# Kernel optimization log

Hardware: AMD Instinct MI355X
Metric: run time of the kernel (lower is better)

## Reference

```python
import jax, jax.numpy as jnp
import numpy as np

N_CENTER, N_NEAR, N_STEPK, N_HOPS = 512, 32, 10, 2
FEAT_NAMES = ["xyz_fea", "pmt_fea", "mad_fea", "dim_fea", "nor_fea", "loc_fea", "fea"]


def pairwise_sqdist(x):
    # x: [B,N,C] -> [B,N,N]
    xx = jnp.sum(x * x, axis=-1)
    return xx[:, :, None] + xx[:, None, :] - 2.0 * jnp.einsum('bnc,bmc->bnm', x, x)


def surface_knn(x, n_near, n_stepk, n_hops=N_HOPS):
    # Iterative surface-KNN: build a step-KNN graph with n_stepk neighbors,
    # expand the neighborhood n_hops times (neighbor-of-neighbor union), then
    # pick the n_near nearest points among the reachable candidate set.
    d = pairwise_sqdist(x)                      # [B,N,N]
    B, N, _ = d.shape
    _, nbr = jax.lax.top_k(-d, n_stepk + 1)     # step neighbors (incl. self)
    b_idx = jnp.arange(B)[:, None, None]
    r_idx = jnp.arange(N)[None, :, None]
    adj = jnp.zeros((B, N, N), jnp.bool_).at[b_idx, r_idx, nbr].set(True)
    reach = adj
    adj_f = adj.astype(jnp.float32)
    for _ in range(n_hops):
        reach = (jnp.einsum('bij,bjk->bik', reach.astype(jnp.float32), adj_f) > 0) | adj
    dm = jnp.where(reach, d, jnp.inf)
    _, idx = jax.lax.top_k(-dm, n_near)         # [B,N,n_near], nearest reachable
    return idx


def fps(x, n_center):
    # Farthest point sampling in the C-dim feature space (dim=dim in source).
    B, N, _ = x.shape
    d = pairwise_sqdist(x)
    barange = jnp.arange(B)

    def step(carry, _):
        mind, prev = carry
        mind = jnp.minimum(mind, d[barange, prev])   # [B,N]
        nxt = jnp.argmax(mind, axis=-1).astype(jnp.int32)
        return (mind, nxt), nxt

    init = (jnp.full((B, N), jnp.inf, jnp.float32), jnp.zeros((B,), jnp.int32))
    _, rest = jax.lax.scan(step, init, None, length=n_center - 1)  # [S-1,B]
    idx = jnp.concatenate([jnp.zeros((1, B), jnp.int32), rest], axis=0)
    return idx.T                                   # [B,S]


def branch(center, grouped, wq, bq, wk, bk, wv, bv, w1, b1, w2, b2):
    # center: [B,S,C], grouped: [B,S,K,C]
    C = center.shape[-1]
    q = center @ wq + bq                           # [B,S,C]
    k = grouped @ wk + bk                          # [B,S,K,C]
    v = grouped @ wv + bv
    scores = jnp.einsum('bsc,bskc->bsk', q, k) / jnp.sqrt(jnp.float32(C))
    attn = jax.nn.softmax(scores, axis=-1)
    out = jnp.einsum('bsk,bskc->bsc', attn, v)     # attention pooling -> [B,S,C]
    h = jax.nn.relu(out @ w1 + b1)                 # MLP (C -> Cout -> Cout)
    return jax.nn.relu(h @ w2 + b2)


def setup_inputs() -> dict:
    key = jax.random.key(0)
    ks = jax.random.split(key, 16)
    B, N, C, CO = 8, 2048, 128, 256
    inp = {}
    for i, name in enumerate(FEAT_NAMES):
        inp[name] = jax.random.normal(ks[i], (B, N, C), jnp.float32)
    s = np.float32(1.0 / np.sqrt(C))
    so = np.float32(1.0 / np.sqrt(CO))
    inp['aw_q'] = jax.random.normal(ks[7], (7, C, C), jnp.float32) * s
    inp['ab_q'] = jnp.zeros((7, C), jnp.float32)
    inp['aw_k'] = jax.random.normal(ks[8], (7, C, C), jnp.float32) * s
    inp['ab_k'] = jnp.zeros((7, C), jnp.float32)
    inp['aw_v'] = jax.random.normal(ks[9], (7, C, C), jnp.float32) * s
    inp['ab_v'] = jnp.zeros((7, C), jnp.float32)
    inp['mw1'] = jax.random.normal(ks[10], (7, C, CO), jnp.float32) * s
    inp['mb1'] = jnp.zeros((7, CO), jnp.float32)
    inp['mw2'] = jax.random.normal(ks[11], (7, CO, CO), jnp.float32) * so
    inp['mb2'] = jnp.zeros((7, CO), jnp.float32)
    return inp


def reference(xyz_fea, pmt_fea, mad_fea, dim_fea, nor_fea, loc_fea, fea,
              aw_q, ab_q, aw_k, ab_k, aw_v, ab_v, mw1, mb1, mw2, mb2):
    B = xyz_fea.shape[0]
    feats = jnp.stack([xyz_fea, pmt_fea, mad_fea, dim_fea, nor_fea, loc_fea, fea], 0)  # [7,B,N,C]
    idx_all = surface_knn(xyz_fea, N_NEAR, N_STEPK)      # [B,N,K]
    fps_idx = fps(xyz_fea, N_CENTER)                     # [B,S]
    b2 = jnp.arange(B)[:, None]                          # [B,1]
    b3 = jnp.arange(B)[:, None, None]                    # [B,1,1]
    centers = feats[:, b2, fps_idx]                      # [7,B,S,C]
    idx = idx_all[b2, fps_idx]                           # [B,S,K]
    grouped = feats[:, b3, idx]                          # [7,B,S,K,C]
    outs = jax.vmap(branch)(centers, grouped, aw_q, ab_q, aw_k, ab_k,
                            aw_v, ab_v, mw1, mb1, mw2, mb2)  # [7,B,S,CO]
    return tuple(outs[i] for i in range(7))
```

## Files before the change

### kernel.cpp

```cpp
#include <hip/hip_runtime.h>
#include <hip/hip_bf16.h>
#include <math.h>

constexpr int BATCH = 8;
constexpr int NPTS  = 2048;
constexpr int CH    = 128;
constexpr int CHO   = 256;
constexpr int NCEN  = 512;
constexpr int NNEI  = 32;
constexpr int NTOP  = 11;
constexpr int NW    = 64;

struct Ptr7 { const float* p[7]; };

__global__ __launch_bounds__(256) void xx_kernel(const float* __restrict__ x,
                                                 float* __restrict__ xx) {
    int p = blockIdx.x * 256 + threadIdx.x;
    if (p >= BATCH * NPTS) return;
    const float4* xr = (const float4*)(x + (size_t)p * CH);
    float s = 0.f;
#pragma unroll
    for (int i = 0; i < CH / 4; i++) {
        float4 v = xr[i];
        s += v.x * v.x + v.y * v.y + v.z * v.z + v.w * v.w;
    }
    xx[p] = s;
}

__global__ __launch_bounds__(256) void dmat_kernel(const float* __restrict__ x,
                                                   const float* __restrict__ xx,
                                                   float* __restrict__ D) {
    __shared__ float As[32][68];
    __shared__ float Bs[32][68];
    int bz = blockIdx.z;
    int i0 = blockIdx.y * 64, j0 = blockIdx.x * 64;
    const float* X = x + (size_t)bz * NPTS * CH;
    int t = threadIdx.x, tx = t & 15, ty = t >> 4;
    int lr = t >> 3, lc = (t & 7) * 4;
    const float* ai0 = X + (size_t)(i0 + lr) * CH;
    const float* ai1 = X + (size_t)(i0 + lr + 32) * CH;
    const float* bj0 = X + (size_t)(j0 + lr) * CH;
    const float* bj1 = X + (size_t)(j0 + lr + 32) * CH;
    float acc[4][4] = {};
    for (int kc = 0; kc < CH; kc += 32) {
        float4 a0 = *(const float4*)(ai0 + kc + lc);
        float4 a1 = *(const float4*)(ai1 + kc + lc);
        float4 b0 = *(const float4*)(bj0 + kc + lc);
        float4 b1 = *(const float4*)(bj1 + kc + lc);
        __syncthreads();
        As[lc + 0][lr] = a0.x; As[lc + 1][lr] = a0.y; As[lc + 2][lr] = a0.z; As[lc + 3][lr] = a0.w;
        As[lc + 0][lr + 32] = a1.x; As[lc + 1][lr + 32] = a1.y; As[lc + 2][lr + 32] = a1.z; As[lc + 3][lr + 32] = a1.w;
        Bs[lc + 0][lr] = b0.x; Bs[lc + 1][lr] = b0.y; Bs[lc + 2][lr] = b0.z; Bs[lc + 3][lr] = b0.w;
        Bs[lc + 0][lr + 32] = b1.x; Bs[lc + 1][lr + 32] = b1.y; Bs[lc + 2][lr + 32] = b1.z; Bs[lc + 3][lr + 32] = b1.w;
        __syncthreads();
#pragma unroll
        for (int kk = 0; kk < 32; kk++) {
            float4 av = *(const float4*)&As[kk][ty * 4];
            float4 bv = *(const float4*)&Bs[kk][tx * 4];
            float a[4] = {av.x, av.y, av.z, av.w};
            float b[4] = {bv.x, bv.y, bv.z, bv.w};
#pragma unroll
            for (int i = 0; i < 4; i++)
#pragma unroll
                for (int j = 0; j < 4; j++) acc[i][j] += a[i] * b[j];
        }
    }
    const float* xxb = xx + bz * NPTS;
    float xi[4], xj[4];
#pragma unroll
    for (int i = 0; i < 4; i++) xi[i] = xxb[i0 + ty * 4 + i];
#pragma unroll
    for (int j = 0; j < 4; j++) xj[j] = xxb[j0 + tx * 4 + j];
#pragma unroll
    for (int i = 0; i < 4; i++) {
        float4 o;
        o.x = xi[i] + xj[0] - 2.f * acc[i][0];
        o.y = xi[i] + xj[1] - 2.f * acc[i][1];
        o.z = xi[i] + xj[2] - 2.f * acc[i][2];
        o.w = xi[i] + xj[3] - 2.f * acc[i][3];
        *(float4*)(D + ((size_t)bz * NPTS + i0 + ty * 4 + i) * NPTS + j0 + tx * 4) = o;
    }
}

__global__ __launch_bounds__(256) void knn_fps_kernel(const float* __restrict__ D,
                                                      unsigned int* __restrict__ adj,
                                                      int* __restrict__ fps_idx) {
    if (blockIdx.x < BATCH) {
        int lane = threadIdx.x;
        if (lane >= 64) return;
        int b = blockIdx.x;
        float mind[32];
#pragma unroll
        for (int r = 0; r < 32; r++) mind[r] = INFINITY;
        int prev = 0;
        if (lane == 0) fps_idx[b * NCEN] = 0;
        const float* Db = D + (size_t)b * NPTS * NPTS;
        for (int s = 1; s < NCEN; s++) {
            const float4* rowp = (const float4*)(Db + (size_t)prev * NPTS);
            float4 v0 = rowp[lane + 0 * 64];
            float4 v1 = rowp[lane + 1 * 64];
            float4 v2 = rowp[lane + 2 * 64];
            float4 v3 = rowp[lane + 3 * 64];
            float4 v4 = rowp[lane + 4 * 64];
            float4 v5 = rowp[lane + 5 * 64];
            float4 v6 = rowp[lane + 6 * 64];
            float4 v7 = rowp[lane + 7 * 64];
            float bv = -INFINITY; int bj = NPTS;
            float4 vv[8] = {v0, v1, v2, v3, v4, v5, v6, v7};
#pragma unroll
            for (int k = 0; k < 8; k++) {
                int j0 = 4 * (lane + 64 * k);
                float m0 = fminf(mind[4 * k + 0], vv[k].x); mind[4 * k + 0] = m0;
                float m1 = fminf(mind[4 * k + 1], vv[k].y); mind[4 * k + 1] = m1;
                float m2 = fminf(mind[4 * k + 2], vv[k].z); mind[4 * k + 2] = m2;
                float m3 = fminf(mind[4 * k + 3], vv[k].w); mind[4 * k + 3] = m3;
                if (m0 > bv) { bv = m0; bj = j0 + 0; }
                if (m1 > bv) { bv = m1; bj = j0 + 1; }
                if (m2 > bv) { bv = m2; bj = j0 + 2; }
                if (m3 > bv) { bv = m3; bj = j0 + 3; }
            }
#pragma unroll
            for (int off = 32; off > 0; off >>= 1) {
                float ov = __shfl_xor(bv, off);
                int oj = __shfl_xor(bj, off);
                if (ov > bv || (ov == bv && oj < bj)) { bv = ov; bj = oj; }
            }
            if (lane == 0) fps_idx[b * NCEN + s] = bj;
            prev = bj;
        }
        return;
    }
    __shared__ float row[NPTS];
    __shared__ float rv[256];
    __shared__ int ri[256];
    __shared__ int picks[NTOP + 1];
    int rid = blockIdx.x - BATCH;
    const float* Dr = D + (size_t)rid * NPTS;
    int t = threadIdx.x;
    float4* rp = (float4*)row;
    rp[t] = ((const float4*)Dr)[t];
    rp[t + 256] = ((const float4*)Dr)[t + 256];
    __syncthreads();
    for (int it = 0; it < NTOP; it++) {
        float bv = row[t];
        int bi = t;
#pragma unroll
        for (int k = 1; k < 8; k++) {
            int j = t + (k << 8);
            float v = row[j];
            if (v < bv) { bv = v; bi = j; }
        }
        rv[t] = bv; ri[t] = bi;
        __syncthreads();
        for (int off = 128; off > 0; off >>= 1) {
            if (t < off) {
                float ov = rv[t + off]; int oi = ri[t + off];
                if (ov < rv[t] || (ov == rv[t] && oi < ri[t])) { rv[t] = ov; ri[t] = oi; }
            }
            __syncthreads();
        }
        if (t == 0) { picks[it] = ri[0]; row[ri[0]] = INFINITY; }
        __syncthreads();
    }
    if (t < NW) {
        unsigned w = 0;
#pragma unroll
        for (int p = 0; p < NTOP; p++) {
            int j = picks[p];
            if ((j >> 5) == t) w |= 1u << (j & 31);
        }
        adj[(size_t)rid * NW + t] = w;
    }
}

__global__ void make_gather(const int* __restrict__ fps_idx, int* __restrict__ gatherC) {
    int r = blockIdx.x * 256 + threadIdx.x;
    if (r >= BATCH * NCEN) return;
    int b = r >> 9, s = r & 511;
    gatherC[r] = b * NPTS + fps_idx[b * NCEN + s];
}

__global__ __launch_bounds__(256) void reach_top32_kernel(const unsigned int* __restrict__ adj,
                                                          const float* __restrict__ D,
                                                          const int* __restrict__ fps_idx,
                                                          int* __restrict__ idx_sel) {
    __shared__ unsigned adjw[NW], R1[NW], R2[NW];
    __shared__ int lst[NPTS];
    __shared__ float dst[NPTS];
    __shared__ int cnt;
    __shared__ float rv[256];
    __shared__ int rj[256], rp[256];
    __shared__ int sel[NNEI];
    int s = blockIdx.x, b = blockIdx.y, t = threadIdx.x;
    int i = fps_idx[b * NCEN + s];
    const unsigned* arow = adj + ((size_t)(b * NPTS + i)) * NW;
    if (t < NW) { adjw[t] = arow[t]; R1[t] = arow[t]; }
    if (t == 0) cnt = 0;
    __syncthreads();
    if (t < NW) {
        unsigned w = adjw[t];
        while (w) { int bb = __ffs(w) - 1; w &= w - 1; int p = atomicAdd(&cnt, 1); lst[p] = t * 32 + bb; }
    }
    __syncthreads();
    int n1 = cnt;
    {
        int g = t >> 6, lane = t & 63;
        for (int p = g; p < n1; p += 4) {
            unsigned aw = adj[((size_t)(b * NPTS + lst[p])) * NW + lane];
            atomicOr(&R1[lane], aw);
        }
    }
    __syncthreads();
    if (t == 0) cnt = 0;
    __syncthreads();
    if (t < NW) {
        unsigned w = R1[t];
        while (w) { int bb = __ffs(w) - 1; w &= w - 1; int p = atomicAdd(&cnt, 1); lst[p] = t * 32 + bb; }
        R2[t] = adjw[t];
    }
    __syncthreads();
    int n2 = cnt;
    {
        int g = t >> 6, lane = t & 63;
        for (int p = g; p < n2; p += 4) {
            unsigned aw = adj[((size_t)(b * NPTS + lst[p])) * NW + lane];
            atomicOr(&R2[lane], aw);
        }
    }
    __syncthreads();
    if (t == 0) cnt = 0;
    __syncthreads();
    const float* Dr = D + (size_t)(b * NPTS + i) * NPTS;
    if (t < NW) {
        unsigned w = R2[t];
        while (w) {
            int bb = __ffs(w) - 1; w &= w - 1;
            int j = t * 32 + bb;
            int p = atomicAdd(&cnt, 1);
            lst[p] = j; dst[p] = Dr[j];
        }
    }
    __syncthreads();
    int L = cnt;
    int nsel = L < NNEI ? L : NNEI;
    for (int r = 0; r < nsel; r++) {
        float bv = INFINITY; int bj = 0x7fffffff, bp = -1;
        for (int p = t; p < L; p += 256) {
            float v = dst[p]; int j = lst[p];
            if (v < bv || (v == bv && j < bj)) { bv = v; bj = j; bp = p; }
        }
        rv[t] = bv; rj[t] = bj; rp[t] = bp;
        __syncthreads();
        for (int off = 128; off > 0; off >>= 1) {
            if (t < off) {
                if (rv[t + off] < rv[t] || (rv[t + off] == rv[t] && rj[t + off] < rj[t])) {
                    rv[t] = rv[t + off]; rj[t] = rj[t + off]; rp[t] = rp[t + off];
                }
            }
            __syncthreads();
        }
        if (t == 0) { sel[r] = rj[0]; dst[rp[0]] = INFINITY; }
        __syncthreads();
    }
    if (t == 0 && nsel < NNEI) {
        int r = nsel;
        for (int j = 0; j < NPTS && r < NNEI; j++)
            if (!((R2[j >> 5] >> (j & 31)) & 1)) sel[r++] = j;
    }
    __syncthreads();
    if (t < NNEI) idx_sel[((size_t)(b * NCEN + s)) * NNEI + t] = sel[t];
}

template <int KSIZE, bool RELU>
__device__ __forceinline__ void gemm_tile64(const float* __restrict__ A, int lda,
                                            const int* __restrict__ gather,
                                            const float* __restrict__ W, int ldw,
                                            const float* __restrict__ bias,
                                            float* __restrict__ Out, int ldo) {
    __shared__ float As[32][68];
    __shared__ float Ws[32][68];
    int t = threadIdx.x;
    int tx = t & 15, ty = t >> 4;
    int lr = t >> 3, lc = (t & 7) * 4;
    const float* ar0 = A + (size_t)(gather ? gather[lr] : lr) * lda;
    const float* ar1 = A + (size_t)(gather ? gather[lr + 32] : lr + 32) * lda;
    float acc[4][4] = {};
    for (int kc = 0; kc < KSIZE; kc += 32) {
        float4 a0 = *(const float4*)(ar0 + kc + lc);
        float4 a1 = *(const float4*)(ar1 + kc + lc);
        float4 w0 = *(const float4*)(W + (size_t)(kc + lr) * ldw + lc);
        float4 w1 = *(const float4*)(W + (size_t)(kc + lr) * ldw + lc + 32);
        __syncthreads();
        As[lc + 0][lr] = a0.x; As[lc + 1][lr] = a0.y; As[lc + 2][lr] = a0.z; As[lc + 3][lr] = a0.w;
        As[lc + 0][lr + 32] = a1.x; As[lc + 1][lr + 32] = a1.y; As[lc + 2][lr + 32] = a1.z; As[lc + 3][lr + 32] = a1.w;
        *(float4*)&Ws[lr][lc] = w0;
        *(float4*)&Ws[lr][lc + 32] = w1;
        __syncthreads();
#pragma unroll
        for (int kk = 0; kk < 32; kk++) {
            float4 av = *(const float4*)&As[kk][ty * 4];
            float4 wv = *(const float4*)&Ws[kk][tx * 4];
            float a[4] = {av.x, av.y, av.z, av.w};
            float w[4] = {wv.x, wv.y, wv.z, wv.w};
#pragma unroll
            for (int i = 0; i < 4; i++)
#pragma unroll
                for (int j = 0; j < 4; j++) acc[i][j] += a[i] * w[j];
        }
    }
#pragma unroll
    for (int i = 0; i < 4; i++) {
        int r = ty * 4 + i;
        float4 o;
        o.x = acc[i][0] + bias[tx * 4 + 0];
        o.y = acc[i][1] + bias[tx * 4 + 1];
        o.z = acc[i][2] + bias[tx * 4 + 2];
        o.w = acc[i][3] + bias[tx * 4 + 3];
        if (RELU) {
            o.x = fmaxf(o.x, 0.f); o.y = fmaxf(o.y, 0.f);
            o.z = fmaxf(o.z, 0.f); o.w = fmaxf(o.w, 0.f);
        }
        *(float4*)(Out + (size_t)r * ldo + tx * 4) = o;
    }
}

__global__ __launch_bounds__(256) void kvproj_kernel(Ptr7 feats, const float* __restrict__ awk,
                                                     const float* __restrict__ abk,
                                                     const float* __restrict__ awv,
                                                     const float* __restrict__ abv,
                                                     float* __restrict__ ktab,
                                                     float* __restrict__ vtab) {
    int v = blockIdx.z, ct = blockIdx.y, rt = blockIdx.x;
    bool isv = ct >= 2;
    int c2 = ct & 1;
    const float* A = feats.p[v] + (size_t)rt * 64 * CH;
    const float* W = (isv ? awv : awk) + (size_t)v * CH * CH + c2 * 64;
    const float* bias = (isv ? abv : abk) + v * CH + c2 * 64;
    float* Out = (isv ? vtab : ktab) + (size_t)v * (BATCH * NPTS) * CH + (size_t)rt * 64 * CH + c2 * 64;
    gemm_tile64<CH, false>(A, CH, nullptr, W, CH, bias, Out, CH);
}

__global__ __launch_bounds__(256) void qproj_kernel(Ptr7 feats, const float* __restrict__ awq,
                                                    const float* __restrict__ abq,
                                                    const int* __restrict__ gatherC,
                                                    float* __restrict__ qtab) {
    int v = blockIdx.z, ct = blockIdx.y, rt = blockIdx.x;
    gemm_tile64<CH, false>(feats.p[v], CH, gatherC + rt * 64,
                           awq + (size_t)v * CH * CH + ct * 64, CH,
                           abq + v * CH + ct * 64,
                           qtab + ((size_t)v * (BATCH * NCEN) + rt * 64) * CH + ct * 64, CH);
}

__global__ __launch_bounds__(256) void mlp1_kernel(const float* __restrict__ otab,
                                                   const float* __restrict__ mw1,
                                                   const float* __restrict__ mb1,
                                                   float* __restrict__ htab) {
    int v = blockIdx.z, ct = blockIdx.y, rt = blockIdx.x;
    gemm_tile64<CH, true>(otab + ((size_t)v * (BATCH * NCEN) + rt * 64) * CH, CH, nullptr,
                          mw1 + (size_t)v * CH * CHO + ct * 64, CHO,
                          mb1 + v * CHO + ct * 64,
                          htab + ((size_t)v * (BATCH * NCEN) + rt * 64) * CHO + ct * 64, CHO);
}

__global__ __launch_bounds__(256) void mlp2_kernel(const float* __restrict__ htab,
                                                   const float* __restrict__ mw2,
                                                   const float* __restrict__ mb2,
                                                   float* __restrict__ out) {
    int v = blockIdx.z, ct = blockIdx.y, rt = blockIdx.x;
    gemm_tile64<CHO, true>(htab + ((size_t)v * (BATCH * NCEN) + rt * 64) * CHO, CHO, nullptr,
                           mw2 + (size_t)v * CHO * CHO + ct * 64, CHO,
                           mb2 + v * CHO + ct * 64,
                           out + ((size_t)v * (BATCH * NCEN) + rt * 64) * CHO + ct * 64, CHO);
}

__global__ __launch_bounds__(256) void attn_kernel(const float* __restrict__ qtab,
                                                   const float* __restrict__ ktab,
                                                   const float* __restrict__ vtab,
                                                   const int* __restrict__ idx_sel,
                                                   float* __restrict__ otab) {
    __shared__ float q_s[4][CH];
    __shared__ float attn_s[4][NNEI];
    __shared__ int jj_s[4][NNEI];
    int v = blockIdx.y;
    int t = threadIdx.x, w = t >> 6, lane = t & 63;
    int cg = blockIdx.x * 4 + w;
    int b = cg >> 9, s = cg & 511;
    const float* qr = qtab + ((size_t)v * (BATCH * NCEN) + cg) * CH;
    *(float2*)&q_s[w][lane * 2] = *(const float2*)(qr + lane * 2);
    if (lane < NNEI) jj_s[w][lane] = idx_sel[((size_t)(b * NCEN + s)) * NNEI + lane];
    __syncthreads();
    if (lane < NNEI) {
        int j = jj_s[w][lane];
        const float* kr = ktab + ((size_t)v * (BATCH * NPTS) + b * NPTS + j) * CH;
        float acc = 0.f;
#pragma unroll
        for (int c4 = 0; c4 < CH / 4; c4++) {
            float4 qv = *(const float4*)&q_s[w][c4 * 4];
            float4 kv = *(const float4*)(kr + c4 * 4);
            acc += qv.x * kv.x + qv.y * kv.y + qv.z * kv.z + qv.w * kv.w;
        }
        float sc = acc * 0.08838834764831845f;
        float m = sc;
#pragma unroll
        for (int off = 16; off > 0; off >>= 1) m = fmaxf(m, __shfl_xor(m, off, 32));
        float e = expf(sc - m);
        float sum = e;
#pragma unroll
        for (int off = 16; off > 0; off >>= 1) sum += __shfl_xor(sum, off, 32);
        attn_s[w][lane] = e / sum;
    }
    __syncthreads();
    float2 o = {0.f, 0.f};
    const float* vbase = vtab + ((size_t)v * (BATCH * NPTS) + b * NPTS) * CH;
    for (int tt = 0; tt < NNEI; tt++) {
        int j = jj_s[w][tt];
        float a = attn_s[w][tt];
        float2 vv = *(const float2*)(vbase + (size_t)j * CH + lane * 2);
        o.x += a * vv.x;
        o.y += a * vv.y;
    }
    *(float2*)(otab + ((size_t)v * (BATCH * NCEN) + cg) * CH + lane * 2) = o;
}

extern "C" void kernel_launch(void* const* d_in, const int* in_sizes, int n_in,
                              void* d_out, int out_size, void* d_ws, size_t ws_size,
                              hipStream_t stream) {
    (void)in_sizes; (void)n_in; (void)out_size;
    Ptr7 feats;
    for (int i = 0; i < 7; i++) feats.p[i] = (const float*)d_in[i];
    const float* awq = (const float*)d_in[7];
    const float* abq = (const float*)d_in[8];
    const float* awk = (const float*)d_in[9];
    const float* abk = (const float*)d_in[10];
    const float* awv = (const float*)d_in[11];
    const float* abv = (const float*)d_in[12];
    const float* mw1 = (const float*)d_in[13];
    const float* mb1 = (const float*)d_in[14];
    const float* mw2 = (const float*)d_in[15];
    const float* mb2 = (const float*)d_in[16];
    const float* xyz = feats.p[0];

    char* ws = (char*)d_ws;
    size_t SZ_D = (size_t)BATCH * NPTS * NPTS * 4;
    float* D = (float*)ws;
    float* ktab = (float*)ws;
    float* vtab = (float*)(ws + (size_t)7 * BATCH * NPTS * CH * 4);
    size_t off = SZ_D;
    float* xx = (float*)(ws + off); off += (size_t)BATCH * NPTS * 4;
    unsigned* adjb = (unsigned*)(ws + off); off += (size_t)BATCH * NPTS * NW * 4;
    int* fpsidx = (int*)(ws + off); off += (size_t)BATCH * NCEN * 4;
    int* idxsel = (int*)(ws + off); off += (size_t)BATCH * NCEN * NNEI * 4;
    int* gatherC = (int*)(ws + off); off += (size_t)BATCH * NCEN * 4;
    float* qtab = (float*)(ws + off); off += (size_t)7 * BATCH * NCEN * CH * 4;
    float* otab = (float*)(ws + off); off += (size_t)7 * BATCH * NCEN * CH * 4;
    float* htab = (float*)(ws + off); off += (size_t)7 * BATCH * NCEN * CHO * 4;
    if (ws_size < off) return;

    xx_kernel<<<dim3((BATCH * NPTS + 255) / 256), dim3(256), 0, stream>>>(xyz, xx);
    dmat_kernel<<<dim3(NPTS / 64, NPTS / 64, BATCH), dim3(256), 0, stream>>>(xyz, xx, D);
    knn_fps_kernel<<<dim3(BATCH + BATCH * NPTS), dim3(256), 0, stream>>>(D, adjb, fpsidx);
    make_gather<<<dim3((BATCH * NCEN + 255) / 256), dim3(256), 0, stream>>>(fpsidx, gatherC);
    reach_top32_kernel<<<dim3(NCEN, BATCH), dim3(256), 0, stream>>>(adjb, D, fpsidx, idxsel);
    kvproj_kernel<<<dim3(BATCH * NPTS / 64, 4, 7), dim3(256), 0, stream>>>(feats, awk, abk, awv, abv, ktab, vtab);
    qproj_kernel<<<dim3(BATCH * NCEN / 64, 2, 7), dim3(256), 0, stream>>>(feats, awq, abq, gatherC, qtab);
    attn_kernel<<<dim3(BATCH * NCEN / 4, 7), dim3(256), 0, stream>>>(qtab, ktab, vtab, idxsel, otab);
    mlp1_kernel<<<dim3(BATCH * NCEN / 64, 4, 7), dim3(256), 0, stream>>>(otab, mw1, mb1, htab);
    mlp2_kernel<<<dim3(BATCH * NCEN / 64, 4, 7), dim3(256), 0, stream>>>(htab, mw2, mb2, (float*)d_out);
}
```

Measured before the change: 1.162 ms.

## Fuse K/V projection into the FPS/KNN kernel to overlap with serial FPS

Adds K/V projection GEMM tiles as extra blocks in the kernel that runs FPS and step-KNN, so the projection work can fill the GPU while the few serial FPS blocks run. Because of this, K/V tables get separate workspace instead of aliasing the distance matrix, with a fallback to the old separate launch when workspace is too small. The FPS min-distance array moves from registers to shared memory, and all GEMMs now use a passed-in shared buffer. Risks: the active path depends on workspace size, and FPS picks up shared-memory traffic on its critical path.

```diff
diff --git a/kernel.cpp b/kernel.cpp
--- a/kernel.cpp
+++ b/kernel.cpp
@@ -10,6 +10,7 @@
 constexpr int NNEI  = 32;
 constexpr int NTOP  = 11;
 constexpr int NW    = 64;
+constexpr int SMEM_BYTES = 17408;
 
 struct Ptr7 { const float* p[7]; };
 
@@ -82,42 +83,108 @@
     }
 }
 
-__global__ __launch_bounds__(256) void knn_fps_kernel(const float* __restrict__ D,
-                                                      unsigned int* __restrict__ adj,
-                                                      int* __restrict__ fps_idx) {
+template <int KSIZE, bool RELU>
+__device__ __forceinline__ void gemm_tile64(char* smem,
+                                            const float* __restrict__ A, int lda,
+                                            const int* __restrict__ gather,
+                                            const float* __restrict__ W, int ldw,
+                                            const float* __restrict__ bias,
+                                            float* __restrict__ Out, int ldo) {
+    float (*As)[68] = (float(*)[68])smem;
+    float (*Ws)[68] = (float(*)[68])(smem + 32 * 68 * 4);
+    int t = threadIdx.x;
+    int tx = t & 15, ty = t >> 4;
+    int lr = t >> 3, lc = (t & 7) * 4;
+    const float* ar0 = A + (size_t)(gather ? gather[lr] : lr) * lda;
+    const float* ar1 = A + (size_t)(gather ? gather[lr + 32] : lr + 32) * lda;
+    float acc[4][4] = {};
+    for (int kc = 0; kc < KSIZE; kc += 32) {
+        float4 a0 = *(const float4*)(ar0 + kc + lc);
+        float4 a1 = *(const float4*)(ar1 + kc + lc);
+        float4 w0 = *(const float4*)(W + (size_t)(kc + lr) * ldw + lc);
+        float4 w1 = *(const float4*)(W + (size_t)(kc + lr) * ldw + lc + 32);
+        __syncthreads();
+        As[lc + 0][lr] = a0.x; As[lc + 1][lr] = a0.y; As[lc + 2][lr] = a0.z; As[lc + 3][lr] = a0.w;
+        As[lc + 0][lr + 32] = a1.x; As[lc + 1][lr + 32] = a1.y; As[lc + 2][lr + 32] = a1.z; As[lc + 3][lr + 32] = a1.w;
+        *(float4*)&Ws[lr][lc] = w0;
+        *(float4*)&Ws[lr][lc + 32] = w1;
+        __syncthreads();
+#pragma unroll
+        for (int kk = 0; kk < 32; kk++) {
+            float4 av = *(const float4*)&As[kk][ty * 4];
+            float4 wv = *(const float4*)&Ws[kk][tx * 4];
+            float a[4] = {av.x, av.y, av.z, av.w};
+            float w[4] = {wv.x, wv.y, wv.z, wv.w};
+#pragma unroll
+            for (int i = 0; i < 4; i++)
+#pragma unroll
+                for (int j = 0; j < 4; j++) acc[i][j] += a[i] * w[j];
+        }
+    }
+#pragma unroll
+    for (int i = 0; i < 4; i++) {
+        int r = ty * 4 + i;
+        float4 o;
+        o.x = acc[i][0] + bias[tx * 4 + 0];
+        o.y = acc[i][1] + bias[tx * 4 + 1];
+        o.z = acc[i][2] + bias[tx * 4 + 2];
+        o.w = acc[i][3] + bias[tx * 4 + 3];
+        if (RELU) {
+            o.x = fmaxf(o.x, 0.f); o.y = fmaxf(o.y, 0.f);
+            o.z = fmaxf(o.z, 0.f); o.w = fmaxf(o.w, 0.f);
+        }
+        *(float4*)(Out + (size_t)r * ldo + tx * 4) = o;
+    }
+}
+
+__global__ __launch_bounds__(256) void fused_front_kernel(const float* __restrict__ D,
+                                                          unsigned int* __restrict__ adj,
+                                                          int* __restrict__ fps_idx,
+                                                          Ptr7 feats,
+                                                          const float* __restrict__ awk,
+                                                          const float* __restrict__ abk,
+                                                          const float* __restrict__ awv,
+                                                          const float* __restrict__ abv,
+                                                          float* __restrict__ ktab,
+                                                          float* __restrict__ vtab) {
+    __shared__ __align__(16) char smem[SMEM_BYTES];
     if (blockIdx.x < BATCH) {
         int lane = threadIdx.x;
         if (lane >= 64) return;
         int b = blockIdx.x;
-        float mind[32];
-#pragma unroll
-        for (int r = 0; r < 32; r++) mind[r] = INFINITY;
+        float4* mp = (float4*)smem;
+        float4 inf4 = {INFINITY, INFINITY, INFINITY, INFINITY};
+#pragma unroll
+        for (int k = 0; k < 8; k++) mp[lane + 64 * k] = inf4;
         int prev = 0;
         if (lane == 0) fps_idx[b * NCEN] = 0;
         const float* Db = D + (size_t)b * NPTS * NPTS;
         for (int s = 1; s < NCEN; s++) {
             const float4* rowp = (const float4*)(Db + (size_t)prev * NPTS);
-            float4 v0 = rowp[lane + 0 * 64];
-            float4 v1 = rowp[lane + 1 * 64];
-            float4 v2 = rowp[lane + 2 * 64];
-            float4 v3 = rowp[lane + 3 * 64];
-            float4 v4 = rowp[lane + 4 * 64];
-            float4 v5 = rowp[lane + 5 * 64];
-            float4 v6 = rowp[lane + 6 * 64];
-            float4 v7 = rowp[lane + 7 * 64];
+            float4 g0 = rowp[lane + 0 * 64];
+            float4 g1 = rowp[lane + 1 * 64];
+            float4 g2 = rowp[lane + 2 * 64];
+            float4 g3 = rowp[lane + 3 * 64];
+            float4 g4 = rowp[lane + 4 * 64];
+            float4 g5 = rowp[lane + 5 * 64];
+            float4 g6 = rowp[lane + 6 * 64];
+            float4 g7 = rowp[lane + 7 * 64];
+            float4 g[8] = {g0, g1, g2, g3, g4, g5, g6, g7};
             float bv = -INFINITY; int bj = NPTS;
-            float4 vv[8] = {v0, v1, v2, v3, v4, v5, v6, v7};
 #pragma unroll
             for (int k = 0; k < 8; k++) {
-                int j0 = 4 * (lane + 64 * k);
-                float m0 = fminf(mind[4 * k + 0], vv[k].x); mind[4 * k + 0] = m0;
-                float m1 = fminf(mind[4 * k + 1], vv[k].y); mind[4 * k + 1] = m1;
-                float m2 = fminf(mind[4 * k + 2], vv[k].z); mind[4 * k + 2] = m2;
-                float m3 = fminf(mind[4 * k + 3], vv[k].w); mind[4 * k + 3] = m3;
-                if (m0 > bv) { bv = m0; bj = j0 + 0; }
-                if (m1 > bv) { bv = m1; bj = j0 + 1; }
-                if (m2 > bv) { bv = m2; bj = j0 + 2; }
-                if (m3 > bv) { bv = m3; bj = j0 + 3; }
+                int li = lane + 64 * k;
+                float4 m = mp[li];
+                m.x = fminf(m.x, g[k].x);
+                m.y = fminf(m.y, g[k].y);
+                m.z = fminf(m.z, g[k].z);
+                m.w = fminf(m.w, g[k].w);
+                mp[li] = m;
+                int j0 = 4 * li;
+                if (m.x > bv) { bv = m.x; bj = j0 + 0; }
+                if (m.y > bv) { bv = m.y; bj = j0 + 1; }
+                if (m.z > bv) { bv = m.z; bj = j0 + 2; }
+                if (m.w > bv) { bv = m.w; bj = j0 + 3; }
             }
 #pragma unroll
             for (int off = 32; off > 0; off >>= 1) {
@@ -130,46 +197,62 @@
         }
         return;
     }
-    __shared__ float row[NPTS];
-    __shared__ float rv[256];
-    __shared__ int ri[256];
-    __shared__ int picks[NTOP + 1];
-    int rid = blockIdx.x - BATCH;
-    const float* Dr = D + (size_t)rid * NPTS;
-    int t = threadIdx.x;
-    float4* rp = (float4*)row;
-    rp[t] = ((const float4*)Dr)[t];
-    rp[t + 256] = ((const float4*)Dr)[t + 256];
-    __syncthreads();
-    for (int it = 0; it < NTOP; it++) {
-        float bv = row[t];
-        int bi = t;
-#pragma unroll
-        for (int k = 1; k < 8; k++) {
-            int j = t + (k << 8);
-            float v = row[j];
-            if (v < bv) { bv = v; bi = j; }
-        }
-        rv[t] = bv; ri[t] = bi;
-        __syncthreads();
-        for (int off = 128; off > 0; off >>= 1) {
-            if (t < off) {
-                float ov = rv[t + off]; int oi = ri[t + off];
-                if (ov < rv[t] || (ov == rv[t] && oi < ri[t])) { rv[t] = ov; ri[t] = oi; }
+    if (blockIdx.x < BATCH + BATCH * NPTS) {
+        float* row = (float*)smem;
+        float* rv = row + NPTS;
+        int* ri = (int*)(rv + 256);
+        int* picks = ri + 256;
+        int rid = blockIdx.x - BATCH;
+        const float* Dr = D + (size_t)rid * NPTS;
+        int t = threadIdx.x;
+        float4* rp = (float4*)row;
+        rp[t] = ((const float4*)Dr)[t];
+        rp[t + 256] = ((const float4*)Dr)[t + 256];
+        __syncthreads();
+        for (int it = 0; it < NTOP; it++) {
+            float bv = row[t];
+            int bi = t;
+#pragma unroll
+            for (int k = 1; k < 8; k++) {
+                int j = t + (k << 8);
+                float v = row[j];
+                if (v < bv) { bv = v; bi = j; }
             }
+            rv[t] = bv; ri[t] = bi;
             __syncthreads();
-        }
-        if (t == 0) { picks[it] = ri[0]; row[ri[0]] = INFINITY; }
-        __syncthreads();
-    }
-    if (t < NW) {
-        unsigned w = 0;
-#pragma unroll
-        for (int p = 0; p < NTOP; p++) {
-            int j = picks[p];
-            if ((j >> 5) == t) w |= 1u << (j & 31);
-        }
-        adj[(size_t)rid * NW + t] = w;
+            for (int off = 128; off > 0; off >>= 1) {
+                if (t < off) {
+                    float ov = rv[t + off]; int oi = ri[t + off];
+                    if (ov < rv[t] || (ov == rv[t] && oi < ri[t])) { rv[t] = ov; ri[t] = oi; }
+                }
+                __syncthreads();
+            }
+            if (t == 0) { picks[it] = ri[0]; row[ri[0]] = INFINITY; }
+            __syncthreads();
+        }
+        if (t < NW) {
+            unsigned w = 0;
+#pragma unroll
+            for (int p = 0; p < NTOP; p++) {
+                int j = picks[p];
+                if ((j >> 5) == t) w |= 1u << (j & 31);
+            }
+            adj[(size_t)rid * NW + t] = w;
+        }
+        return;
+    }
+    {
+        int id = blockIdx.x - BATCH - BATCH * NPTS;
+        int rt = id & 255;
+        int ct = (id >> 8) & 3;
+        int v = id >> 10;
+        bool isv = ct >= 2;
+        int c2 = ct & 1;
+        const float* A = feats.p[v] + (size_t)rt * 64 * CH;
+        const float* W = (isv ? awv : awk) + (size_t)v * CH * CH + c2 * 64;
+        const float* bias = (isv ? abv : abk) + v * CH + c2 * 64;
+        float* Out = (isv ? vtab : ktab) + (size_t)v * (BATCH * NPTS) * CH + (size_t)rt * 64 * CH + c2 * 64;
+        gemm_tile64<CH, false>(smem, A, CH, nullptr, W, CH, bias, Out, CH);
     }
 }
 
@@ -271,65 +354,13 @@
     if (t < NNEI) idx_sel[((size_t)(b * NCEN + s)) * NNEI + t] = sel[t];
 }
 
-template <int KSIZE, bool RELU>
-__device__ __forceinline__ void gemm_tile64(const float* __restrict__ A, int lda,
-                                            const int* __restrict__ gather,
-                                            const float* __restrict__ W, int ldw,
-                                            const float* __restrict__ bias,
-                                            float* __restrict__ Out, int ldo) {
-    __shared__ float As[32][68];
-    __shared__ float Ws[32][68];
-    int t = threadIdx.x;
-    int tx = t & 15, ty = t >> 4;
-    int lr = t >> 3, lc = (t & 7) * 4;
-    const float* ar0 = A + (size_t)(gather ? gather[lr] : lr) * lda;
-    const float* ar1 = A + (size_t)(gather ? gather[lr + 32] : lr + 32) * lda;
-    float acc[4][4] = {};
-    for (int kc = 0; kc < KSIZE; kc += 32) {
-        float4 a0 = *(const float4*)(ar0 + kc + lc);
-        float4 a1 = *(const float4*)(ar1 + kc + lc);
-        float4 w0 = *(const float4*)(W + (size_t)(kc + lr) * ldw + lc);
-        float4 w1 = *(const float4*)(W + (size_t)(kc + lr) * ldw + lc + 32);
-        __syncthreads();
-        As[lc + 0][lr] = a0.x; As[lc + 1][lr] = a0.y; As[lc + 2][lr] = a0.z; As[lc + 3][lr] = a0.w;
-        As[lc + 0][lr + 32] = a1.x; As[lc + 1][lr + 32] = a1.y; As[lc + 2][lr + 32] = a1.z; As[lc + 3][lr + 32] = a1.w;
-        *(float4*)&Ws[lr][lc] = w0;
-        *(float4*)&Ws[lr][lc + 32] = w1;
-        __syncthreads();
-#pragma unroll
-        for (int kk = 0; kk < 32; kk++) {
-            float4 av = *(const float4*)&As[kk][ty * 4];
-            float4 wv = *(const float4*)&Ws[kk][tx * 4];
-            float a[4] = {av.x, av.y, av.z, av.w};
-            float w[4] = {wv.x, wv.y, wv.z, wv.w};
-#pragma unroll
-            for (int i = 0; i < 4; i++)
-#pragma unroll
-                for (int j = 0; j < 4; j++) acc[i][j] += a[i] * w[j];
-        }
-    }
-#pragma unroll
-    for (int i = 0; i < 4; i++) {
-        int r = ty * 4 + i;
-        float4 o;
-        o.x = acc[i][0] + bias[tx * 4 + 0];
-        o.y = acc[i][1] + bias[tx * 4 + 1];
-        o.z = acc[i][2] + bias[tx * 4 + 2];
-        o.w = acc[i][3] + bias[tx * 4 + 3];
-        if (RELU) {
-            o.x = fmaxf(o.x, 0.f); o.y = fmaxf(o.y, 0.f);
-            o.z = fmaxf(o.z, 0.f); o.w = fmaxf(o.w, 0.f);
-        }
-        *(float4*)(Out + (size_t)r * ldo + tx * 4) = o;
-    }
-}
-
 __global__ __launch_bounds__(256) void kvproj_kernel(Ptr7 feats, const float* __restrict__ awk,
                                                      const float* __restrict__ abk,
                                                      const float* __restrict__ awv,
                                                      const float* __restrict__ abv,
                                                      float* __restrict__ ktab,
                                                      float* __restrict__ vtab) {
+    __shared__ __align__(16) char smem[SMEM_BYTES];
     int v = blockIdx.z, ct = blockIdx.y, rt = blockIdx.x;
     bool isv = ct >= 2;
     int c2 = ct & 1;
@@ -337,15 +368,16 @@
     const float* W = (isv ? awv : awk) + (size_t)v * CH * CH + c2 * 64;
     const float* bias = (isv ? abv : abk) + v * CH + c2 * 64;
     float* Out = (isv ? vtab : ktab) + (size_t)v * (BATCH * NPTS) * CH + (size_t)rt * 64 * CH + c2 * 64;
-    gemm_tile64<CH, false>(A, CH, nullptr, W, CH, bias, Out, CH);
+    gemm_tile64<CH, false>(smem, A, CH, nullptr, W, CH, bias, Out, CH);
 }
 
 __global__ __launch_bounds__(256) void qproj_kernel(Ptr7 feats, const float* __restrict__ awq,
                                                     const float* __restrict__ abq,
                                                     const int* __restrict__ gatherC,
                                                     float* __restrict__ qtab) {
+    __shared__ __align__(16) char smem[SMEM_BYTES];
     int v = blockIdx.z, ct = blockIdx.y, rt = blockIdx.x;
-    gemm_tile64<CH, false>(feats.p[v], CH, gatherC + rt * 64,
+    gemm_tile64<CH, false>(smem, feats.p[v], CH, gatherC + rt * 64,
                            awq + (size_t)v * CH * CH + ct * 64, CH,
                            abq + v * CH + ct * 64,
                            qtab + ((size_t)v * (BATCH * NCEN) + rt * 64) * CH + ct * 64, CH);
@@ -355,8 +387,9 @@
                                                    const float* __restrict__ mw1,
                                                    const float* __restrict__ mb1,
                                                    float* __restrict__ htab) {
+    __shared__ __align__(16) char smem[SMEM_BYTES];
     int v = blockIdx.z, ct = blockIdx.y, rt = blockIdx.x;
-    gemm_tile64<CH, true>(otab + ((size_t)v * (BATCH * NCEN) + rt * 64) * CH, CH, nullptr,
+    gemm_tile64<CH, true>(smem, otab + ((size_t)v * (BATCH * NCEN) + rt * 64) * CH, CH, nullptr,
                           mw1 + (size_t)v * CH * CHO + ct * 64, CHO,
                           mb1 + v * CHO + ct * 64,
                           htab + ((size_t)v * (BATCH * NCEN) + rt * 64) * CHO + ct * 64, CHO);
@@ -366,8 +399,9 @@
                                                    const float* __restrict__ mw2,
                                                    const float* __restrict__ mb2,
                                                    float* __restrict__ out) {
+    __shared__ __align__(16) char smem[SMEM_BYTES];
     int v = blockIdx.z, ct = blockIdx.y, rt = blockIdx.x;
-    gemm_tile64<CHO, true>(htab + ((size_t)v * (BATCH * NCEN) + rt * 64) * CHO, CHO, nullptr,
+    gemm_tile64<CHO, true>(smem, htab + ((size_t)v * (BATCH * NCEN) + rt * 64) * CHO, CHO, nullptr,
                            mw2 + (size_t)v * CHO * CHO + ct * 64, CHO,
                            mb2 + v * CHO + ct * 64,
                            out + ((size_t)v * (BATCH * NCEN) + rt * 64) * CHO + ct * 64, CHO);
@@ -442,9 +476,8 @@
 
     char* ws = (char*)d_ws;
     size_t SZ_D = (size_t)BATCH * NPTS * NPTS * 4;
+    size_t SZ_KV = (size_t)7 * BATCH * NPTS * CH * 4;
     float* D = (float*)ws;
-    float* ktab = (float*)ws;
-    float* vtab = (float*)(ws + (size_t)7 * BATCH * NPTS * CH * 4);
     size_t off = SZ_D;
     float* xx = (float*)(ws + off); off += (size_t)BATCH * NPTS * 4;
     unsigned* adjb = (unsigned*)(ws + off); off += (size_t)BATCH * NPTS * NW * 4;
@@ -455,13 +488,25 @@
     float* otab = (float*)(ws + off); off += (size_t)7 * BATCH * NCEN * CH * 4;
     float* htab = (float*)(ws + off); off += (size_t)7 * BATCH * NCEN * CHO * 4;
     if (ws_size < off) return;
+    bool kv_sep = (ws_size >= off + 2 * SZ_KV);
+    float *ktab, *vtab;
+    if (kv_sep) {
+        ktab = (float*)(ws + off); off += SZ_KV;
+        vtab = (float*)(ws + off); off += SZ_KV;
+    } else {
+        ktab = (float*)ws;
+        vtab = (float*)(ws + SZ_KV);
+    }
 
     xx_kernel<<<dim3((BATCH * NPTS + 255) / 256), dim3(256), 0, stream>>>(xyz, xx);
     dmat_kernel<<<dim3(NPTS / 64, NPTS / 64, BATCH), dim3(256), 0, stream>>>(xyz, xx, D);
-    knn_fps_kernel<<<dim3(BATCH + BATCH * NPTS), dim3(256), 0, stream>>>(D, adjb, fpsidx);
+    int fused_blocks = BATCH + BATCH * NPTS + (kv_sep ? 7 * 4 * (BATCH * NPTS / 64) : 0);
+    fused_front_kernel<<<dim3(fused_blocks), dim3(256), 0, stream>>>(D, adjb, fpsidx, feats,
+                                                                     awk, abk, awv, abv, ktab, vtab);
     make_gather<<<dim3((BATCH * NCEN + 255) / 256), dim3(256), 0, stream>>>(fpsidx, gatherC);
     reach_top32_kernel<<<dim3(NCEN, BATCH), dim3(256), 0, stream>>>(adjb, D, fpsidx, idxsel);
-    kvproj_kernel<<<dim3(BATCH * NPTS / 64, 4, 7), dim3(256), 0, stream>>>(feats, awk, abk, awv, abv, ktab, vtab);
+    if (!kv_sep)
+        kvproj_kernel<<<dim3(BATCH * NPTS / 64, 4, 7), dim3(256), 0, stream>>>(feats, awk, abk, awv, abv, ktab, vtab);
     qproj_kernel<<<dim3(BATCH * NCEN / 64, 2, 7), dim3(256), 0, stream>>>(feats, awq, abq, gatherC, qtab);
     attn_kernel<<<dim3(BATCH * NCEN / 4, 7), dim3(256), 0, stream>>>(qtab, ktab, vtab, idxsel, otab);
     mlp1_kernel<<<dim3(BATCH * NCEN / 64, 4, 7), dim3(256), 0, stream>>>(otab, mw1, mb1, htab);
```

Result: no change. 1.152 ms (-0.8%).
